# Optimization experiments

Hardware: AMD Instinct MI355X
Metric: run time of the kernel (lower is better)

Reference implementation:

```python
import jax, jax.numpy as jnp
import numpy as np

N_NODES = 10000
N_EDGES = 320000
NODE_F = 64
EDGE_F = 32
H = 256
L = 6
HEADS = 8
OUT = H // HEADS
N_GRAPHS = 16
NEG_SLOPE = 0.2  # PyG GATConv leaky_relu slope


def setup_inputs() -> dict:
    key = jax.random.key(0)
    ks = jax.random.split(key, 32)
    s = 0.05
    f32 = jnp.float32
    inp = {}
    inp["x"] = jax.random.normal(ks[0], (N_NODES, NODE_F), f32)
    inp["edge_index"] = jax.random.randint(ks[1], (2, N_EDGES), 0, N_NODES)
    inp["edge_attr"] = jax.random.normal(ks[2], (N_EDGES, EDGE_F), f32)
    inp["batch"] = jnp.sort(jax.random.randint(ks[3], (N_NODES,), 0, N_GRAPHS))
    # embeddings
    inp["node_w"] = jax.random.normal(ks[4], (H, NODE_F), f32) * s
    inp["node_b"] = jnp.zeros((H,), f32)
    inp["edge_emb_w"] = jax.random.normal(ks[5], (H, EDGE_F), f32) * s
    inp["edge_emb_b"] = jnp.zeros((H,), f32)
    # stacked GATConv params (shared lin for src/dst since in_channels is int)
    inp["lin_w"] = jax.random.normal(ks[6], (L, H, H), f32) * s
    inp["att_src"] = jax.random.normal(ks[7], (L, HEADS, OUT), f32) * s
    inp["att_dst"] = jax.random.normal(ks[8], (L, HEADS, OUT), f32) * s
    inp["att_edge"] = jax.random.normal(ks[9], (L, HEADS, OUT), f32) * s
    inp["lin_edge_w"] = jax.random.normal(ks[10], (L, H, H), f32) * s
    inp["conv_b"] = jnp.zeros((L, H), f32)
    inp["ln_g"] = jnp.ones((L, H), f32)
    inp["ln_b"] = jnp.zeros((L, H), f32)
    # MLP heads: Linear(2H->H), Linear(H->H/2), Linear(H/2->3)
    inp["pw1"] = jax.random.normal(ks[11], (H, 2 * H), f32) * s
    inp["pb1"] = jnp.zeros((H,), f32)
    inp["pw2"] = jax.random.normal(ks[12], (H // 2, H), f32) * s
    inp["pb2"] = jnp.zeros((H // 2,), f32)
    inp["pw3"] = jax.random.normal(ks[13], (3, H // 2), f32) * s
    inp["pb3"] = jnp.zeros((3,), f32)
    inp["mw1"] = jax.random.normal(ks[14], (H, 2 * H), f32) * s
    inp["mb1"] = jnp.zeros((H,), f32)
    inp["mw2"] = jax.random.normal(ks[15], (H // 2, H), f32) * s
    inp["mb2"] = jnp.zeros((H // 2,), f32)
    inp["mw3"] = jax.random.normal(ks[16], (3, H // 2), f32) * s
    inp["mb3"] = jnp.zeros((3,), f32)
    return inp


def _ln(x, g, b):
    mu = jnp.mean(x, -1, keepdims=True)
    var = jnp.mean(jnp.square(x - mu), -1, keepdims=True)
    return g * (x - mu) * jax.lax.rsqrt(var + 1e-5) + b


def _mlp(z, w1, b1, w2, b2, w3, b3):
    h = jax.nn.gelu(z @ w1.T + b1, approximate=False)
    h = jax.nn.gelu(h @ w2.T + b2, approximate=False)
    return jax.nn.sigmoid(h @ w3.T + b3)


def _gnn_forward(x, edge_attr, src, dst, batch,
                 node_w, node_b, edge_emb_w, edge_emb_b,
                 lin_w, att_src, att_dst, att_edge, lin_edge_w, conv_b,
                 ln_g, ln_b,
                 pw1, pb1, pw2, pb2, pw3, pb3,
                 mw1, mb1, mw2, mb2, mw3, mb3):
    h = x @ node_w.T + node_b                       # [N, H]
    ea = edge_attr @ edge_emb_w.T + edge_emb_b      # [E, H]
    # PyG add_self_loops(fill_value='mean'): loop attr = mean of incoming edge attrs
    cnt = jax.ops.segment_sum(jnp.ones((N_EDGES,), h.dtype), dst, N_NODES)
    loop_attr = jax.ops.segment_sum(ea, dst, N_NODES) / jnp.maximum(cnt, 1.0)[:, None]
    ea_full = jnp.concatenate([ea, loop_attr], 0)   # [E+N, H]
    loops = jnp.arange(N_NODES, dtype=src.dtype)
    src_f = jnp.concatenate([src, loops])
    dst_f = jnp.concatenate([dst, loops])
    for i in range(L):
        x_in = h
        xw = (h @ lin_w[i].T).reshape(N_NODES, HEADS, OUT)
        eap = (ea_full @ lin_edge_w[i].T).reshape(-1, HEADS, OUT)
        a_src = jnp.sum(xw * att_src[i], -1)        # [N, heads]
        a_dst = jnp.sum(xw * att_dst[i], -1)
        alpha = a_src[src_f] + a_dst[dst_f] + jnp.sum(eap * att_edge[i], -1)  # [E+N, heads]
        alpha = jnp.where(alpha > 0, alpha, NEG_SLOPE * alpha)
        amax = jax.ops.segment_max(alpha, dst_f, N_NODES)
        e = jnp.exp(alpha - amax[dst_f])
        denom = jax.ops.segment_sum(e, dst_f, N_NODES)
        w = e / (denom[dst_f] + 1e-16)
        msg = xw[src_f] * w[:, :, None]             # [E+N, heads, out]
        hi = jax.ops.segment_sum(msg, dst_f, N_NODES).reshape(N_NODES, H) + conv_b[i]
        hi = jax.nn.gelu(_ln(hi, ln_g[i], ln_b[i]), approximate=False)
        h = hi + x_in if i > 0 else hi
    sums = jax.ops.segment_sum(h, batch, N_GRAPHS)  # [G, H]
    ncnt = jax.ops.segment_sum(jnp.ones((N_NODES,), h.dtype), batch, N_GRAPHS)
    mean = sums / jnp.maximum(ncnt, 1.0)[:, None]
    xg = jnp.concatenate([mean, sums], 1)           # [G, 2H]
    params = _mlp(xg, pw1, pb1, pw2, pb2, pw3, pb3)
    metrics = _mlp(xg, mw1, mb1, mw2, mb2, mw3, mb3)
    return params, metrics


def reference(x, edge_index, edge_attr, batch,
              node_w, node_b, edge_emb_w, edge_emb_b,
              lin_w, att_src, att_dst, att_edge, lin_edge_w, conv_b,
              ln_g, ln_b,
              pw1, pb1, pw2, pb2, pw3, pb3,
              mw1, mb1, mw2, mb2, mw3, mb3):
    return _gnn_forward(x, edge_attr, edge_index[0], edge_index[1], batch,
                        node_w, node_b, edge_emb_w, edge_emb_b,
                        lin_w, att_src, att_dst, att_edge, lin_edge_w, conv_b,
                        ln_g, ln_b,
                        pw1, pb1, pw2, pb2, pw3, pb3,
                        mw1, mb1, mw2, mb2, mw3, mb3)
```

## Files before the change

kernel.cpp:

```cpp
#include <hip/hip_runtime.h>
#include <math.h>

#define NN 10000
#define NE 320000
#define NODE_F 64
#define EDGE_F 32
#define HDIM 256
#define HEADS 8
#define LAYERS 6
#define NG 16
#define NOUT 48
#define LOG2E 1.4426950408889634f

typedef __attribute__((ext_vector_type(8))) short short8;
typedef __attribute__((ext_vector_type(4))) float float4v;
typedef __attribute__((ext_vector_type(2))) float floatx2;

__global__ void scan_kernel(const int* __restrict__ cnt, int* __restrict__ row_ptr,
                            int* __restrict__ pos) {
    __shared__ int wsum[16];
    __shared__ int woff[16];
    int t = threadIdx.x;
    int lane = t & 63, wid = t >> 6;
    const int chunk = 10;
    int lo = t * chunk;
    int loc[10];
    int s = 0;
    #pragma unroll
    for (int k = 0; k < 10; ++k) {
        int i = lo + k;
        int v = (i < NN) ? cnt[i] : 0;
        loc[k] = v;
        s += v;
    }
    int inc = s;
    #pragma unroll
    for (int off = 1; off < 64; off <<= 1) {
        int v = __shfl_up(inc, off, 64);
        if (lane >= off) inc += v;
    }
    if (lane == 63) wsum[wid] = inc;
    __syncthreads();
    if (t < 16) {
        int inc2 = wsum[t];
        #pragma unroll
        for (int off = 1; off < 16; off <<= 1) {
            int u = __shfl_up(inc2, off, 16);
            if (t >= off) inc2 += u;
        }
        woff[t] = inc2;
    }
    __syncthreads();
    int base = inc - s + (wid ? woff[wid - 1] : 0);
    #pragma unroll
    for (int k = 0; k < 10; ++k) {
        int i = lo + k;
        if (i < NN) {
            row_ptr[i] = base;
            pos[i] = base;
            base += loc[k];
        }
    }
    if (t == 1023) row_ptr[NN] = woff[15];
}

__global__ void scatter_kernel(const int* __restrict__ src, const int* __restrict__ dst,
                               int* __restrict__ pos, int2* __restrict__ csr_se) {
    int e = blockIdx.x * 256 + threadIdx.x;
    if (e >= NE) return;
    int d = dst[e];
    int idx = atomicAdd(&pos[d], 1);
    csr_se[idx] = make_int2(src[e], e);
}

__device__ __forceinline__ ushort f2bf(float f) {
    union { float f; unsigned u; } v; v.f = f;
    unsigned u = v.u;
    return (ushort)((u + 0x7fffu + ((u >> 16) & 1u)) >> 16);
}
__device__ __forceinline__ float bf2f(ushort b) {
    union { unsigned u; float f; } v; v.u = ((unsigned)b) << 16; return v.f;
}

__global__ __launch_bounds__(256) void prep_kernel(const float* __restrict__ att_edge,
                                                   const float* __restrict__ lin_edge_w,
                                                   const float* __restrict__ eew,
                                                   const float* __restrict__ eeb,
                                                   ushort* __restrict__ webbf,
                                                   float* __restrict__ bebuf) {
    int ih = blockIdx.x;
    int i = ih >> 3, h = ih & 7;
    __shared__ float vsh[HDIM];
    int t = threadIdx.x;
    float s = 0.f;
    const float* ae = att_edge + ih * 32;
    const float* lw = lin_edge_w + ((size_t)i * HDIM + h * 32) * HDIM + t;
    #pragma unroll
    for (int o = 0; o < 32; ++o) s += ae[o] * lw[(size_t)o * HDIM];
    vsh[t] = s;
    __syncthreads();
    if (t < EDGE_F) {
        float acc = 0.f;
        for (int k = 0; k < HDIM; ++k) acc += vsh[k] * eew[k * EDGE_F + t];
        webbf[ih * EDGE_F + t] = f2bf(acc * LOG2E);
    } else if (t == EDGE_F) {
        float acc = 0.f;
        for (int k = 0; k < HDIM; ++k) acc += vsh[k] * eeb[k];
        bebuf[ih] = acc * LOG2E;
    }
}

__global__ __launch_bounds__(64) void fold0_kernel(const float* __restrict__ lin_w,
                                                   const float* __restrict__ node_w,
                                                   const float* __restrict__ node_b,
                                                   ushort* __restrict__ w0p,
                                                   float* __restrict__ b0p) {
    int j = blockIdx.x, f = threadIdx.x;
    const float* wr = lin_w + (size_t)j * HDIM;
    float acc = 0.f, accb = 0.f;
    for (int k = 0; k < HDIM; ++k) acc += wr[k] * node_w[k * NODE_F + f];
    #pragma unroll
    for (int m = 0; m < 4; ++m) {
        int k = f + 64 * m;
        accb += wr[k] * node_b[k];
    }
    w0p[j * NODE_F + f] = f2bf(acc);
    #pragma unroll
    for (int off = 32; off >= 1; off >>= 1) accb += __shfl_xor(accb, off, 64);
    if (f == 0) b0p[j] = accb;
}

__global__ __launch_bounds__(256) void preE_kernel(const float* __restrict__ edge_attr,
                                                   const ushort* __restrict__ web,
                                                   const float* __restrict__ be,
                                                   ushort* __restrict__ preEb,
                                                   const int* __restrict__ dst,
                                                   int* __restrict__ cnt) {
    int t = threadIdx.x;
    if (t < 64) atomicAdd(&cnt[dst[blockIdx.x * 64 + t]], 1);
    int wv = t >> 6, l = t & 63;
    int base = blockIdx.x * 64 + wv * 16;
    int m = l & 15, kq = (l >> 4) * 8;
    const float* ar = edge_attr + (size_t)(base + m) * EDGE_F + kq;
    float4 a0 = *(const float4*)(ar);
    float4 a1 = *(const float4*)(ar + 4);
    short8 afrag;
    afrag[0] = (short)f2bf(a0.x); afrag[1] = (short)f2bf(a0.y);
    afrag[2] = (short)f2bf(a0.z); afrag[3] = (short)f2bf(a0.w);
    afrag[4] = (short)f2bf(a1.x); afrag[5] = (short)f2bf(a1.y);
    afrag[6] = (short)f2bf(a1.z); afrag[7] = (short)f2bf(a1.w);
    float4v zero = {0.f, 0.f, 0.f, 0.f};
    float4v acc[3];
    #pragma unroll
    for (int ct = 0; ct < 3; ++ct) {
        short8 bfrag = *(const short8*)(web + (size_t)(ct * 16 + m) * EDGE_F + kq);
        acc[ct] = __builtin_amdgcn_mfma_f32_16x16x32_bf16(afrag, bfrag, zero, 0, 0, 0);
    }
    #pragma unroll
    for (int ct = 0; ct < 3; ++ct) {
        int oc = ct * 16 + m;
        int li = oc >> 3, hh = oc & 7;
        float bv = be[oc];
        #pragma unroll
        for (int r = 0; r < 4; ++r) {
            int row = (l >> 4) * 4 + r;
            preEb[(size_t)li * NE * 8 + (size_t)(base + row) * 8 + hh] = f2bf(acc[ct][r] + bv);
        }
    }
}

__global__ void tobf_all_kernel(const float* __restrict__ lin_w,
                                const float* __restrict__ x, ushort* __restrict__ wbhi,
                                ushort* __restrict__ xhi) {
    const int N1 = LAYERS * HDIM * HDIM;
    const int N2 = N1 + NN * NODE_F;
    int i = blockIdx.x * 256 + threadIdx.x;
    if (i < N1) wbhi[i] = f2bf(lin_w[i]);
    else if (i < N2) xhi[i - N1] = f2bf(x[i - N1]);
}

__global__ __launch_bounds__(128) void gemm_bf1(const ushort* __restrict__ Ah,
                                                const ushort* __restrict__ Bh,
                                                const float* __restrict__ bias,
                                                unsigned char* __restrict__ Cf8,
                                                const float* __restrict__ att_s,
                                                const float* __restrict__ att_d,
                                                float* __restrict__ a_src,
                                                float* __restrict__ a_dst,
                                                int N, int K) {
    __shared__ ushort sAh[64][40], sBh[64][40];
    int nb = blockIdx.y * 64, jb = blockIdx.x * 64;
    int t = threadIdx.x, w = t >> 6, l = t & 63;
    int srow = t >> 1, sq = (t & 1) * 16;
    int fr = l & 15, fq = (l >> 4) * 8;
    float4v acc[2][4] = {};
    for (int kt = 0; kt < K; kt += 32) {
        int gr = nb + srow;
        short8 a0 = {0,0,0,0,0,0,0,0}, a1 = {0,0,0,0,0,0,0,0};
        if (gr < N) {
            const short8* pa = (const short8*)(Ah + (size_t)gr * K + kt + sq);
            a0 = pa[0]; a1 = pa[1];
        }
        *(short8*)&sAh[srow][sq] = a0; *(short8*)&sAh[srow][sq + 8] = a1;
        const short8* pb = (const short8*)(Bh + (size_t)(jb + srow) * K + kt + sq);
        short8 b0 = pb[0], b1 = pb[1];
        *(short8*)&sBh[srow][sq] = b0; *(short8*)&sBh[srow][sq + 8] = b1;
        __syncthreads();
        short8 bh[4];
        #pragma unroll
        for (int nt = 0; nt < 4; ++nt)
            bh[nt] = *(const short8*)&sBh[nt * 16 + fr][fq];
        #pragma unroll
        for (int mt = 0; mt < 2; ++mt) {
            short8 ah = *(const short8*)&sAh[w * 32 + mt * 16 + fr][fq];
            #pragma unroll
            for (int nt = 0; nt < 4; ++nt)
                acc[mt][nt] = __builtin_amdgcn_mfma_f32_16x16x32_bf16(ah, bh[nt], acc[mt][nt], 0, 0, 0);
        }
        __syncthreads();
    }
    if (bias) {
        #pragma unroll
        for (int nt = 0; nt < 4; ++nt) {
            float bv = bias[jb + nt * 16 + fr];
            #pragma unroll
            for (int mt = 0; mt < 2; ++mt)
                #pragma unroll
                for (int r = 0; r < 4; ++r) acc[mt][nt][r] += bv;
        }
    }
    #pragma unroll
    for (int mt = 0; mt < 2; ++mt) {
        #pragma unroll
        for (int nt = 0; nt < 4; ++nt) {
            int col = jb + nt * 16 + fr;
            #pragma unroll
            for (int r = 0; r < 4; ++r) {
                int row = nb + w * 32 + mt * 16 + (l >> 4) * 4 + r;
                if (row < N) {
                    float v = acc[mt][nt][r];
                    int pk8 = __builtin_amdgcn_cvt_pk_fp8_f32(v, v, 0, false);
                    Cf8[(size_t)row * HDIM + col] = (unsigned char)(pk8 & 0xff);
                }
            }
        }
    }
    {
        int head0 = jb >> 5;
        float cs[4], cd[4];
        #pragma unroll
        for (int nt = 0; nt < 4; ++nt) {
            cs[nt] = att_s[jb + nt * 16 + fr] * LOG2E;
            cd[nt] = att_d[jb + nt * 16 + fr] * LOG2E;
        }
        #pragma unroll
        for (int mt = 0; mt < 2; ++mt) {
            #pragma unroll
            for (int r = 0; r < 4; ++r) {
                float s0 = acc[mt][0][r] * cs[0] + acc[mt][1][r] * cs[1];
                float s1 = acc[mt][2][r] * cs[2] + acc[mt][3][r] * cs[3];
                float d0 = acc[mt][0][r] * cd[0] + acc[mt][1][r] * cd[1];
                float d1 = acc[mt][2][r] * cd[2] + acc[mt][3][r] * cd[3];
                #pragma unroll
                for (int off = 8; off >= 1; off >>= 1) {
                    s0 += __shfl_xor(s0, off, 16);
                    s1 += __shfl_xor(s1, off, 16);
                    d0 += __shfl_xor(d0, off, 16);
                    d1 += __shfl_xor(d1, off, 16);
                }
                if (fr == 0) {
                    int row = nb + w * 32 + mt * 16 + (l >> 4) * 4 + r;
                    if (row < N) {
                        a_src[row * 8 + head0]     = s0;
                        a_src[row * 8 + head0 + 1] = s1;
                        a_dst[row * 8 + head0]     = d0;
                        a_dst[row * 8 + head0 + 1] = d1;
                    }
                }
            }
        }
    }
}

__device__ __forceinline__ float gelu_exact(float x) {
    return 0.5f * x * (1.f + erff(x * 0.70710678118654752f));
}

__global__ __launch_bounds__(128) void node_kernel(const unsigned char* __restrict__ xwf8,
                                                  const ushort* __restrict__ pb,
                                                  const float* __restrict__ a_src,
                                                  const float* __restrict__ a_dst,
                                                  const int* __restrict__ row_ptr,
                                                  const int2* __restrict__ csr_se,
                                                  const ushort* __restrict__ hp,
                                                  ushort* __restrict__ hout,
                                                  const float* __restrict__ cb,
                                                  const float* __restrict__ lg,
                                                  const float* __restrict__ lb, int first) {
    __shared__ float red[6][128];
    int t = threadIdx.x;
    int wv = t >> 6, l = t & 63;
    int n = blockIdx.x;
    int start = row_ptr[n], end = row_ptr[n + 1];
    int hc = l >> 3;
    int hc8 = l & 56;
    int jj = l & 7;
    float adnh = a_dst[n * 8 + hc];
    const unsigned char* xb = xwf8 + 4 * l;

    float den = 0.f, acc[4] = {0.f, 0.f, 0.f, 0.f};
    float psum = 0.f;
    for (int idx = start + wv * 8; idx < end; idx += 16) {
        int myi = idx + jj;
        bool valid = myi < end;
        int2 se = valid ? csr_se[myi] : make_int2(n, 0);
        int snj[8];
        #pragma unroll
        for (int j = 0; j < 8; ++j) snj[j] = __shfl(se.x, hc8 + j, 64);
        unsigned g[8];
        #pragma unroll
        for (int j = 0; j < 8; ++j) g[j] = *(const unsigned*)(xb + (size_t)snj[j] * HDIM);
        float w_t = 0.f;
        if (valid) {
            float p_t = bf2f(pb[(size_t)se.y * 8 + hc]);
            float a_t = a_src[(size_t)se.x * 8 + hc] + adnh + p_t;
            w_t = exp2f(fminf(fmaxf(a_t, 0.2f * a_t), 57.7f));
            psum += p_t;
        }
        #pragma unroll
        for (int j = 0; j < 8; ++j) {
            float wj = __shfl(w_t, hc8 + j, 64);
            floatx2 lo = __builtin_amdgcn_cvt_pk_f32_fp8(g[j], false);
            floatx2 hi = __builtin_amdgcn_cvt_pk_f32_fp8(g[j], true);
            den += wj;
            acc[0] += wj * lo.x;
            acc[1] += wj * lo.y;
            acc[2] += wj * hi.x;
            acc[3] += wj * hi.y;
        }
    }
    #pragma unroll
    for (int off = 1; off < 8; off <<= 1) psum += __shfl_xor(psum, off, 64);
    red[0][t] = den; red[1][t] = acc[0]; red[2][t] = acc[1];
    red[3][t] = acc[2]; red[4][t] = acc[3]; red[5][t] = psum;
    __syncthreads();
    int ot = t ^ 64;
    den += red[0][ot]; acc[0] += red[1][ot]; acc[1] += red[2][ot];
    acc[2] += red[3][ot]; acc[3] += red[4][ot]; psum += red[5][ot];

    int deg = end - start;
    float preLv = deg > 0 ? psum / (float)deg : 0.f;
    {
        float al = a_src[n * 8 + hc] + adnh + preLv;
        al = fminf(fmaxf(al, 0.2f * al), 57.7f);
        float wself = exp2f(al);
        den += wself;
        unsigned gs = *(const unsigned*)(xb + (size_t)n * HDIM);
        floatx2 lo = __builtin_amdgcn_cvt_pk_f32_fp8(gs, false);
        floatx2 hi = __builtin_amdgcn_cvt_pk_f32_fp8(gs, true);
        acc[0] += wself * lo.x;
        acc[1] += wself * lo.y;
        acc[2] += wself * hi.x;
        acc[3] += wself * hi.y;
    }
    float4 cb4 = *(const float4*)(cb + 4 * l);
    float invh = 1.f / (den + 1e-16f);
    acc[0] = acc[0] * invh + cb4.x;
    acc[1] = acc[1] * invh + cb4.y;
    acc[2] = acc[2] * invh + cb4.z;
    acc[3] = acc[3] * invh + cb4.w;

    float part = acc[0] + acc[1] + acc[2] + acc[3];
    #pragma unroll
    for (int off = 32; off >= 1; off >>= 1) part += __shfl_xor(part, off, 64);
    float mu = part * (1.f / 256.f);
    float p2 = 0.f;
    #pragma unroll
    for (int j = 0; j < 4; ++j) {
        float d = acc[j] - mu;
        p2 += d * d;
    }
    #pragma unroll
    for (int off = 32; off >= 1; off >>= 1) p2 += __shfl_xor(p2, off, 64);
    float rstd = rsqrtf(p2 * (1.f / 256.f) + 1e-5f);

    if (wv == 0) {
        float4 lg4 = *(const float4*)(lg + 4 * l);
        float4 lb4 = *(const float4*)(lb + 4 * l);
        float o4[4];
        float lgv[4] = {lg4.x, lg4.y, lg4.z, lg4.w};
        float lbv[4] = {lb4.x, lb4.y, lb4.z, lb4.w};
        float hpv[4] = {0.f, 0.f, 0.f, 0.f};
        if (!first) {
            uint2 ph = *(const uint2*)(hp + (size_t)n * HDIM + 4 * l);
            hpv[0] = bf2f((ushort)(ph.x & 0xffff));
            hpv[1] = bf2f((ushort)(ph.x >> 16));
            hpv[2] = bf2f((ushort)(ph.y & 0xffff));
            hpv[3] = bf2f((ushort)(ph.y >> 16));
        }
        #pragma unroll
        for (int j = 0; j < 4; ++j) {
            float y = (acc[j] - mu) * rstd * lgv[j] + lbv[j];
            o4[j] = gelu_exact(y) + hpv[j];
        }
        uint2 po;
        po.x = (unsigned)f2bf(o4[0]) | ((unsigned)f2bf(o4[1]) << 16);
        po.y = (unsigned)f2bf(o4[2]) | ((unsigned)f2bf(o4[3]) << 16);
        *(uint2*)(hout + (size_t)n * HDIM + 4 * l) = po;
    }
}

__global__ __launch_bounds__(256) void graph_sum_kernel(const ushort* __restrict__ h,
                                                        const int* __restrict__ batch,
                                                        float* __restrict__ sums) {
    int t = threadIdx.x;
    int n0 = blockIdx.x * 64;
    int n1 = min(NN, n0 + 64);
    float acc = 0.f;
    int cur = batch[n0];
    for (int n = n0; n < n1; ++n) {
        int b = batch[n];
        if (b != cur) {
            atomicAdd(&sums[cur * HDIM + t], acc);
            acc = 0.f;
            cur = b;
        }
        acc += bf2f(h[(size_t)n * HDIM + t]);
    }
    atomicAdd(&sums[cur * HDIM + t], acc);
}

__device__ __forceinline__ int lower_bound_dev(const int* a, int n, int v) {
    int lo = 0, hi = n;
    while (lo < hi) {
        int mid = (lo + hi) >> 1;
        if (a[mid] < v) lo = mid + 1; else hi = mid;
    }
    return lo;
}

__global__ __launch_bounds__(256) void mlp_kernel(const float* __restrict__ sums,
                                                  const int* __restrict__ batch,
                                                  const float* __restrict__ pw1,
                                                  const float* __restrict__ pb1,
                                                  const float* __restrict__ pw2,
                                                  const float* __restrict__ pb2,
                                                  const float* __restrict__ pw3,
                                                  const float* __restrict__ pb3,
                                                  const float* __restrict__ mw1,
                                                  const float* __restrict__ mb1,
                                                  const float* __restrict__ mw2,
                                                  const float* __restrict__ mb2,
                                                  const float* __restrict__ mw3,
                                                  const float* __restrict__ mb3,
                                                  float* __restrict__ out) {
    int g = blockIdx.x, which = blockIdx.y;
    const float* w1 = which ? mw1 : pw1; const float* b1 = which ? mb1 : pb1;
    const float* w2 = which ? mw2 : pw2; const float* b2 = which ? mb2 : pb2;
    const float* w3 = which ? mw3 : pw3; const float* b3 = which ? mb3 : pb3;
    __shared__ float xg[512];
    __shared__ float h1[256];
    __shared__ float h2[128];
    __shared__ float cinv_s;
    int t = threadIdx.x;
    if (t == 0) {
        int s0 = lower_bound_dev(batch, NN, g), s1 = lower_bound_dev(batch, NN, g + 1);
        cinv_s = 1.f / fmaxf((float)(s1 - s0), 1.f);
    }
    __syncthreads();
    float sv = sums[g * HDIM + t];
    xg[t] = sv * cinv_s;
    xg[256 + t] = sv;
    __syncthreads();
    {
        const float* wr = w1 + (size_t)t * 512;
        float acc = 0.f;
        #pragma unroll 8
        for (int k = 0; k < 512; k += 4) {
            float4 wv = *(const float4*)(wr + k);
            acc += wv.x * xg[k] + wv.y * xg[k + 1] + wv.z * xg[k + 2] + wv.w * xg[k + 3];
        }
        h1[t] = gelu_exact(acc + b1[t]);
    }
    __syncthreads();
    {
        int row = t >> 1, hf = t & 1;
        const float* wr = w2 + (size_t)row * 256 + hf * 128;
        const float* hx = h1 + hf * 128;
        float acc = 0.f;
        #pragma unroll 8
        for (int k = 0; k < 128; k += 4) {
            float4 wv = *(const float4*)(wr + k);
            acc += wv.x * hx[k] + wv.y * hx[k + 1] + wv.z * hx[k + 2] + wv.w * hx[k + 3];
        }
        acc += __shfl_xor(acc, 1, 64);
        if (hf == 0) h2[row] = gelu_exact(acc + b2[row]);
    }
    __syncthreads();
    if (t < 64) {
        float v0 = h2[t], v1 = h2[64 + t];
        #pragma unroll
        for (int o = 0; o < 3; ++o) {
            float p = w3[o * 128 + t] * v0 + w3[o * 128 + 64 + t] * v1;
            #pragma unroll
            for (int off = 32; off >= 1; off >>= 1) p += __shfl_xor(p, off, 64);
            if (t == 0) out[which * (NG * 3) + g * 3 + o] = 1.f / (1.f + expf(-(p + b3[o])));
        }
    }
}

extern "C" void kernel_launch(void* const* d_in, const int* in_sizes, int n_in, void* d_out,
                              int out_size, void* d_ws, size_t ws_size, hipStream_t stream) {
    const float* x         = (const float*)d_in[0];
    const int*   ei        = (const int*)d_in[1];
    const int*   src       = ei;
    const int*   dst       = ei + NE;
    const float* edge_attr = (const float*)d_in[2];
    const int*   batch     = (const int*)d_in[3];
    const float* node_w    = (const float*)d_in[4];
    const float* node_b    = (const float*)d_in[5];
    const float* eew       = (const float*)d_in[6];
    const float* eeb       = (const float*)d_in[7];
    const float* lin_w     = (const float*)d_in[8];
    const float* att_src   = (const float*)d_in[9];
    const float* att_dst   = (const float*)d_in[10];
    const float* att_edge  = (const float*)d_in[11];
    const float* lin_edge_w= (const float*)d_in[12];
    const float* conv_b    = (const float*)d_in[13];
    const float* ln_g      = (const float*)d_in[14];
    const float* ln_b      = (const float*)d_in[15];
    const float* pw1 = (const float*)d_in[16]; const float* pb1 = (const float*)d_in[17];
    const float* pw2 = (const float*)d_in[18]; const float* pb2 = (const float*)d_in[19];
    const float* pw3 = (const float*)d_in[20]; const float* pb3 = (const float*)d_in[21];
    const float* mw1 = (const float*)d_in[22]; const float* mb1 = (const float*)d_in[23];
    const float* mw2 = (const float*)d_in[24]; const float* mb2 = (const float*)d_in[25];
    const float* mw3 = (const float*)d_in[26]; const float* mb3 = (const float*)d_in[27];
    float* out = (float*)d_out;

    float* wsf = (float*)d_ws;
    float* a_src     = wsf; wsf += (size_t)NN * HEADS;
    float* a_dst     = wsf; wsf += (size_t)NN * HEADS;
    float* bebuf     = wsf; wsf += 64;
    float* b0p       = wsf; wsf += HDIM;
    ushort* ubuf = (ushort*)wsf;
    ushort* preEb = ubuf; ubuf += (size_t)NE * NOUT;
    ushort* webbf = ubuf; ubuf += (size_t)NOUT * EDGE_F;
    ushort* hb0  = ubuf; ubuf += (size_t)NN * HDIM;
    ushort* hb1  = ubuf; ubuf += (size_t)NN * HDIM;
    unsigned char* xwf8 = (unsigned char*)ubuf; ubuf += (size_t)NN * HDIM / 2;
    ushort* wbhi = ubuf; ubuf += (size_t)LAYERS * HDIM * HDIM;
    ushort* xhi  = ubuf; ubuf += (size_t)NN * NODE_F;
    ushort* w0p  = ubuf; ubuf += (size_t)HDIM * NODE_F;
    int* ibuf    = (int*)ubuf;
    int* cnt     = ibuf; ibuf += NN + 16;
    float* sums  = (float*)ibuf; ibuf += NG * HDIM;
    int* row_ptr = ibuf; ibuf += NN + 16;
    int* pos     = ibuf; ibuf += NN + 16;
    int2* csr_se = (int2*)ibuf; ibuf += 2 * NE;

    hipMemsetAsync(cnt, 0, (NN + 16 + NG * HDIM) * sizeof(int), stream);

    prep_kernel<<<LAYERS * HEADS, 256, 0, stream>>>(att_edge, lin_edge_w, eew, eeb, webbf, bebuf);
    preE_kernel<<<NE / 64, 256, 0, stream>>>(edge_attr, webbf, bebuf, preEb, dst, cnt);

    scan_kernel<<<1, 1024, 0, stream>>>(cnt, row_ptr, pos);
    scatter_kernel<<<(NE + 255) / 256, 256, 0, stream>>>(src, dst, pos, csr_se);

    {
        const int total = LAYERS * HDIM * HDIM + NN * NODE_F;
        tobf_all_kernel<<<(total + 255) / 256, 256, 0, stream>>>(lin_w, x, wbhi, xhi);
    }
    fold0_kernel<<<HDIM, 64, 0, stream>>>(lin_w, node_w, node_b, w0p, b0p);

    ushort* hb[2] = {hb0, hb1};
    for (int i = 0; i < LAYERS; ++i) {
        dim3 grid(HDIM / 64, (NN + 63) / 64);
        const ushort* Ain = (i == 0) ? xhi : hb[(i - 1) & 1];
        const ushort* Bin = (i == 0) ? w0p : wbhi + (size_t)i * HDIM * HDIM;
        int Kin = (i == 0) ? NODE_F : HDIM;
        const float* bias = (i == 0) ? b0p : nullptr;
        gemm_bf1<<<grid, 128, 0, stream>>>(Ain, Bin, bias, xwf8,
                                           att_src + i * HEADS * 32, att_dst + i * HEADS * 32,
                                           a_src, a_dst, NN, Kin);
        node_kernel<<<NN, 128, 0, stream>>>(
            xwf8, preEb + (size_t)i * NE * 8, a_src, a_dst,
            row_ptr, csr_se, (i == 0) ? nullptr : hb[(i - 1) & 1], hb[i & 1],
            conv_b + i * HDIM, ln_g + i * HDIM, ln_b + i * HDIM, i == 0 ? 1 : 0);
    }

    graph_sum_kernel<<<(NN + 63) / 64, 256, 0, stream>>>(hb[(LAYERS - 1) & 1], batch, sums);
    {
        dim3 gm(NG, 2);
        mlp_kernel<<<gm, 256, 0, stream>>>(sums, batch, pw1, pb1, pw2, pb2, pw3, pb3,
                                           mw1, mb1, mw2, mb2, mw3, mb3, out);
    }
}
```

Measured before the change: 473.0 us.

## Store edge attention logits in fp8 and fuse graph pooling into MLP

```diff
diff --git a/kernel.cpp b/kernel.cpp
--- a/kernel.cpp
+++ b/kernel.cpp
@@ -133,7 +133,7 @@
 __global__ __launch_bounds__(256) void preE_kernel(const float* __restrict__ edge_attr,
                                                    const ushort* __restrict__ web,
                                                    const float* __restrict__ be,
-                                                   ushort* __restrict__ preEb,
+                                                   unsigned char* __restrict__ preE8,
                                                    const int* __restrict__ dst,
                                                    int* __restrict__ cnt) {
     int t = threadIdx.x;
@@ -164,7 +164,10 @@
         #pragma unroll
         for (int r = 0; r < 4; ++r) {
             int row = (l >> 4) * 4 + r;
-            preEb[(size_t)li * NE * 8 + (size_t)(base + row) * 8 + hh] = f2bf(acc[ct][r] + bv);
+            float v = acc[ct][r] + bv;
+            int pk8 = __builtin_amdgcn_cvt_pk_fp8_f32(v, v, 0, false);
+            preE8[(size_t)li * NE * 8 + (size_t)(base + row) * 8 + hh] =
+                (unsigned char)(pk8 & 0xff);
         }
     }
 }
@@ -287,7 +290,7 @@
 }
 
 __global__ __launch_bounds__(128) void node_kernel(const unsigned char* __restrict__ xwf8,
-                                                  const ushort* __restrict__ pb,
+                                                  const unsigned char* __restrict__ pb,
                                                   const float* __restrict__ a_src,
                                                   const float* __restrict__ a_dst,
                                                   const int* __restrict__ row_ptr,
@@ -322,7 +325,9 @@
         for (int j = 0; j < 8; ++j) g[j] = *(const unsigned*)(xb + (size_t)snj[j] * HDIM);
         float w_t = 0.f;
         if (valid) {
-            float p_t = bf2f(pb[(size_t)se.y * 8 + hc]);
+            unsigned pu = pb[(size_t)se.y * 8 + hc];
+            floatx2 pd = __builtin_amdgcn_cvt_pk_f32_fp8(pu, false);
+            float p_t = pd.x;
             float a_t = a_src[(size_t)se.x * 8 + hc] + adnh + p_t;
             w_t = exp2f(fminf(fmaxf(a_t, 0.2f * a_t), 57.7f));
             psum += p_t;
@@ -410,26 +415,6 @@
     }
 }
 
-__global__ __launch_bounds__(256) void graph_sum_kernel(const ushort* __restrict__ h,
-                                                        const int* __restrict__ batch,
-                                                        float* __restrict__ sums) {
-    int t = threadIdx.x;
-    int n0 = blockIdx.x * 64;
-    int n1 = min(NN, n0 + 64);
-    float acc = 0.f;
-    int cur = batch[n0];
-    for (int n = n0; n < n1; ++n) {
-        int b = batch[n];
-        if (b != cur) {
-            atomicAdd(&sums[cur * HDIM + t], acc);
-            acc = 0.f;
-            cur = b;
-        }
-        acc += bf2f(h[(size_t)n * HDIM + t]);
-    }
-    atomicAdd(&sums[cur * HDIM + t], acc);
-}
-
 __device__ __forceinline__ int lower_bound_dev(const int* a, int n, int v) {
     int lo = 0, hi = n;
     while (lo < hi) {
@@ -439,7 +424,7 @@
     return lo;
 }
 
-__global__ __launch_bounds__(256) void mlp_kernel(const float* __restrict__ sums,
+__global__ __launch_bounds__(256) void mlp_kernel(const ushort* __restrict__ h,
                                                   const int* __restrict__ batch,
                                                   const float* __restrict__ pw1,
                                                   const float* __restrict__ pb1,
@@ -461,15 +446,12 @@
     __shared__ float xg[512];
     __shared__ float h1[256];
     __shared__ float h2[128];
-    __shared__ float cinv_s;
     int t = threadIdx.x;
-    if (t == 0) {
-        int s0 = lower_bound_dev(batch, NN, g), s1 = lower_bound_dev(batch, NN, g + 1);
-        cinv_s = 1.f / fmaxf((float)(s1 - s0), 1.f);
-    }
-    __syncthreads();
-    float sv = sums[g * HDIM + t];
-    xg[t] = sv * cinv_s;
+    int s0 = lower_bound_dev(batch, NN, g), s1 = lower_bound_dev(batch, NN, g + 1);
+    float sv = 0.f;
+    for (int n = s0; n < s1; ++n) sv += bf2f(h[(size_t)n * HDIM + t]);
+    float cinv = 1.f / fmaxf((float)(s1 - s0), 1.f);
+    xg[t] = sv * cinv;
     xg[256 + t] = sv;
     __syncthreads();
     {
@@ -543,25 +525,26 @@
     float* bebuf     = wsf; wsf += 64;
     float* b0p       = wsf; wsf += HDIM;
     ushort* ubuf = (ushort*)wsf;
-    ushort* preEb = ubuf; ubuf += (size_t)NE * NOUT;
     ushort* webbf = ubuf; ubuf += (size_t)NOUT * EDGE_F;
     ushort* hb0  = ubuf; ubuf += (size_t)NN * HDIM;
     ushort* hb1  = ubuf; ubuf += (size_t)NN * HDIM;
-    unsigned char* xwf8 = (unsigned char*)ubuf; ubuf += (size_t)NN * HDIM / 2;
     ushort* wbhi = ubuf; ubuf += (size_t)LAYERS * HDIM * HDIM;
     ushort* xhi  = ubuf; ubuf += (size_t)NN * NODE_F;
     ushort* w0p  = ubuf; ubuf += (size_t)HDIM * NODE_F;
-    int* ibuf    = (int*)ubuf;
+    unsigned char* cbuf = (unsigned char*)ubuf;
+    unsigned char* preE8 = cbuf; cbuf += (size_t)NE * NOUT;
+    unsigned char* xwf8  = cbuf; cbuf += (size_t)NN * HDIM;
+    cbuf += ((size_t)cbuf & 7) ? (8 - ((size_t)cbuf & 7)) : 0;
+    int* ibuf    = (int*)cbuf;
     int* cnt     = ibuf; ibuf += NN + 16;
-    float* sums  = (float*)ibuf; ibuf += NG * HDIM;
     int* row_ptr = ibuf; ibuf += NN + 16;
     int* pos     = ibuf; ibuf += NN + 16;
     int2* csr_se = (int2*)ibuf; ibuf += 2 * NE;
 
-    hipMemsetAsync(cnt, 0, (NN + 16 + NG * HDIM) * sizeof(int), stream);
+    hipMemsetAsync(cnt, 0, (NN + 16) * sizeof(int), stream);
 
     prep_kernel<<<LAYERS * HEADS, 256, 0, stream>>>(att_edge, lin_edge_w, eew, eeb, webbf, bebuf);
-    preE_kernel<<<NE / 64, 256, 0, stream>>>(edge_attr, webbf, bebuf, preEb, dst, cnt);
+    preE_kernel<<<NE / 64, 256, 0, stream>>>(edge_attr, webbf, bebuf, preE8, dst, cnt);
 
     scan_kernel<<<1, 1024, 0, stream>>>(cnt, row_ptr, pos);
     scatter_kernel<<<(NE + 255) / 256, 256, 0, stream>>>(src, dst, pos, csr_se);
@@ -583,15 +566,15 @@
                                            att_src + i * HEADS * 32, att_dst + i * HEADS * 32,
                                            a_src, a_dst, NN, Kin);
         node_kernel<<<NN, 128, 0, stream>>>(
-            xwf8, preEb + (size_t)i * NE * 8, a_src, a_dst,
+            xwf8, preE8 + (size_t)i * NE * 8, a_src, a_dst,
             row_ptr, csr_se, (i == 0) ? nullptr : hb[(i - 1) & 1], hb[i & 1],
             conv_b + i * HDIM, ln_g + i * HDIM, ln_b + i * HDIM, i == 0 ? 1 : 0);
     }
 
-    graph_sum_kernel<<<(NN + 63) / 64, 256, 0, stream>>>(hb[(LAYERS - 1) & 1], batch, sums);
     {
         dim3 gm(NG, 2);
-        mlp_kernel<<<gm, 256, 0, stream>>>(sums, batch, pw1, pb1, pw2, pb2, pw3, pb3,
+        mlp_kernel<<<gm, 256, 0, stream>>>(hb[(LAYERS - 1) & 1], batch,
+                                           pw1, pb1, pw2, pb2, pw3, pb3,
                                            mw1, mb1, mw2, mb2, mw3, mb3, out);
     }
 }
```

After: 588.2 us. 24.3% more time.
